# Optimization experiments

Measured on AMD Instinct MI355X. Metric: run time of the kernel, lower is better.

## Reference

```python
import jax, jax.numpy as jnp
import numpy as np

B, Q, K, H = 4, 128, 1024, 256
QS, KS, DV = 256, 256, 256


def setup_inputs() -> dict:
    key = jax.random.key(0)
    k1, k2, k3, k4, k5, k6, k7 = jax.random.split(key, 7)
    return {
        "queries": jax.random.normal(k1, (B, Q, QS), dtype=jnp.float32),
        "keys": jax.random.normal(k2, (B, K, KS), dtype=jnp.float32),
        "values": jax.random.normal(k3, (B, K, DV), dtype=jnp.float32),
        "valid_lens": jax.random.randint(k4, (B,), 1, K, dtype=jnp.int64),
        "Wq": jax.random.normal(k5, (QS, H), dtype=jnp.float32) / np.sqrt(QS),
        "Wk": jax.random.normal(k6, (KS, H), dtype=jnp.float32) / np.sqrt(KS),
        "Wv": jax.random.normal(k7, (H,), dtype=jnp.float32) / np.sqrt(H),
    }


def reference(queries, keys, values, valid_lens, Wq, Wk, Wv):
    # Projections: [B,Q,H] and [B,K,H]
    q = jnp.einsum("bqe,eh->bqh", queries, Wq)
    k = jnp.einsum("bke,eh->bkh", keys, Wk)
    # Broadcast add + tanh: [B,Q,K,H] intermediate (the kernel-headroom op)
    feats = jnp.tanh(q[:, :, None, :] + k[:, None, :, :])
    # hidden -> 1 reduction: scores [B,Q,K]
    scores = jnp.einsum("bqkh,h->bqk", feats, Wv)
    # masked softmax: positions >= valid_len set to -1e6 (as in sequence_mask)
    mask = jnp.arange(scores.shape[-1])[None, None, :] < valid_lens[:, None, None]
    scores = jnp.where(mask, scores, jnp.float32(-1e6))
    attn = jax.nn.softmax(scores, axis=-1)
    # dropout is identity in eval mode
    return jnp.einsum("bqk,bkv->bqv", attn, values)
```

## Files before the change

### kernel.cpp

```cpp
#include <hip/hip_runtime.h>

#define NB 4
#define NQ 128
#define NK 1024
#define NH 256
#define NE 256
#define NV 256

#define TSCALE     2.8853900817779268f
#define NEG2LOG2E -2.8853900817779268f

static __device__ __forceinline__ float fexp2(float x){ return __builtin_amdgcn_exp2f(x); }
static __device__ __forceinline__ float frcp (float x){ return __builtin_amdgcn_rcpf(x); }
static __device__ __forceinline__ float expT(float x){ return fexp2(x * TSCALE); }

__global__ __launch_bounds__(256) void proj_kernel(
    const float* __restrict__ qin, const float* __restrict__ kin,
    const float* __restrict__ Wq, const float* __restrict__ Wk,
    float4* __restrict__ qEa, float4* __restrict__ kEt) {
    const int tid = threadIdx.x;
    const int bi  = blockIdx.x;
    __shared__ float tr[NH][5];
    if (bi < NB * 32) {
        const int row0 = bi * 4;
        const float* r0 = qin + row0 * NE;
        float a0 = 0.f, a1 = 0.f, a2 = 0.f, a3 = 0.f;
#pragma unroll 2
        for (int e = 0; e < NE; e += 4) {
            float4 q0 = *(const float4*)(r0 + e);
            float4 q1 = *(const float4*)(r0 + NE + e);
            float4 q2 = *(const float4*)(r0 + 2 * NE + e);
            float4 q3 = *(const float4*)(r0 + 3 * NE + e);
#pragma unroll
            for (int j = 0; j < 4; ++j) {
                float w = Wq[(e + j) * NH + tid];
                a0 = fmaf(((const float*)&q0)[j], w, a0);
                a1 = fmaf(((const float*)&q1)[j], w, a1);
                a2 = fmaf(((const float*)&q2)[j], w, a2);
                a3 = fmaf(((const float*)&q3)[j], w, a3);
            }
        }
        qEa[bi * NH + tid] = make_float4(expT(a0), expT(a1),
                                         expT(a2), expT(a3));
    } else {
        const int kb = bi - NB * 32;
        const int b  = kb >> 8;
        const int k0 = (kb & 255) * 4;
        const int c   = k0 >> 6;
        const int kl0 = k0 & 63;
        const float* kr = kin + (b * NK + k0) * NE;
        float acc[4] = {0.f,0.f,0.f,0.f};
#pragma unroll 2
        for (int e = 0; e < NE; e += 4) {
            float4 kvv[4];
#pragma unroll
            for (int i = 0; i < 4; ++i) kvv[i] = *(const float4*)(kr + i * NE + e);
#pragma unroll
            for (int j = 0; j < 4; ++j) {
                float w = Wk[(e + j) * NH + tid];
#pragma unroll
                for (int i = 0; i < 4; ++i)
                    acc[i] = fmaf(((const float*)&kvv[i])[j], w, acc[i]);
            }
        }
#pragma unroll
        for (int i = 0; i < 4; ++i) tr[tid][i] = expT(acc[i]);
        __syncthreads();
        {
            const int hg = tid >> 2;
            const int kk = tid & 3;
            float4 v = make_float4(tr[hg*4+0][kk], tr[hg*4+1][kk],
                                   tr[hg*4+2][kk], tr[hg*4+3][kk]);
            kEt[((b * 16 + c) * 64 + hg) * 64 + kl0 + kk] = v;
        }
    }
}

__global__ __launch_bounds__(256) void attn_kernel(
    const float4* __restrict__ qEa,
    const float4* __restrict__ kEt, const float* __restrict__ V,
    const int* __restrict__ vlen, const float4* __restrict__ Wv4,
    float* __restrict__ part_s, float* __restrict__ part_pv) {
    const int tid = threadIdx.x, lane = tid & 63, wvid = tid >> 6;
    const int n0 = (vlen[0] + 63) >> 6, n1 = (vlen[1] + 63) >> 6;
    const int n2 = (vlen[2] + 63) >> 6, n3 = (vlen[3] + 63) >> 6;
    const int G  = n0 + n1 + n2 + n3;
    const int bi = blockIdx.x;
    const int xcd = bi & 7;
    const int jj  = bi >> 3;
    const int qq  = jj & 31;
    const int gs  = ((jj >> 5) << 3) + xcd;
    if (gs >= G) return;
    int b, chunk;
    if      (gs < n0)           { b = 0; chunk = gs; }
    else if (gs < n0 + n1)      { b = 1; chunk = gs - n0; }
    else if (gs < n0 + n1 + n2) { b = 2; chunk = gs - n0 - n1; }
    else                        { b = 3; chunk = gs - n0 - n1 - n2; }
    const int vl    = vlen[b];
    const int k0    = chunk * 64;
    const int k     = k0 + lane;
    const int pidx  = (b * 32 + qq) * 16 + chunk;
    float* ps  = part_s + pidx * 4;
    float* ppv = part_pv + pidx * (4 * NV);

    __shared__ float red17[4][64 * 17];
    __shared__ float pwT[64][4];

    const float4* kp = kEt + ((b * 16 + chunk) * 64 + wvid * 16) * 64 + lane;
    const float4* qp = qEa + (b * 32 + qq) * NH;
    float acc0 = 0.f, acc1 = 0.f, acc2 = 0.f, acc3 = 0.f;
#pragma unroll
    for (int i = 0; i < 16; ++i) {
        float4 kv4 = kp[i * 64];
        const int h4 = wvid * 16 + i;
        float4 wv4 = Wv4[h4];
#pragma unroll
        for (int j = 0; j < 4; ++j) {
            float kv  = (j==0)?kv4.x:(j==1)?kv4.y:(j==2)?kv4.z:kv4.w;
            float wvj = (j==0)?wv4.x:(j==1)?wv4.y:(j==2)?wv4.z:wv4.w;
            float4 qa = qp[h4 * 4 + j];
            float t0 = fmaf(qa.x, kv, 1.0f);
            float t1 = fmaf(qa.y, kv, 1.0f);
            float t2 = fmaf(qa.z, kv, 1.0f);
            float t3 = fmaf(qa.w, kv, 1.0f);
            float ab = t0 * t1, cd = t2 * t3;
            float rw = wvj * frcp(ab * cd);
            float rab = rw * cd, rcd = rw * ab;
            acc0 = fmaf(rab, t1, acc0);
            acc1 = fmaf(rab, t0, acc1);
            acc2 = fmaf(rcd, t3, acc2);
            acc3 = fmaf(rcd, t2, acc3);
        }
    }
    {
        float* hp = &red17[wvid][lane * 17];
        hp[0] = acc0; hp[1] = acc1; hp[2] = acc2; hp[3] = acc3;
    }
    __syncthreads();
    {
        const int row = wvid;
        float s = red17[0][lane * 17 + row] + red17[1][lane * 17 + row]
                + red17[2][lane * 17 + row] + red17[3][lane * 17 + row];
        float x = s * NEG2LOG2E;
        x = (k < vl) ? x : -1e38f;
        float p = fexp2(x);
        float u = p;
#pragma unroll
        for (int d = 32; d >= 1; d >>= 1) u += __shfl_xor(u, d, 64);
        if (lane == 0) ps[row] = u;
        pwT[lane][row] = p;
    }
    __syncthreads();
    {
        const float* Vb = V + (b * NK + k0) * NV;
        const int v4 = lane * 4;
        float4 o0 = {0,0,0,0}, o1 = {0,0,0,0}, o2 = {0,0,0,0}, o3 = {0,0,0,0};
#pragma unroll 4
        for (int kk = 0; kk < 16; ++kk) {
            const int kkk = wvid * 16 + kk;
            float4 pv = *(const float4*)&pwT[kkk][0];
            float4 vv = *(const float4*)&Vb[kkk * NV + v4];
            o0.x = fmaf(pv.x, vv.x, o0.x); o0.y = fmaf(pv.x, vv.y, o0.y);
            o0.z = fmaf(pv.x, vv.z, o0.z); o0.w = fmaf(pv.x, vv.w, o0.w);
            o1.x = fmaf(pv.y, vv.x, o1.x); o1.y = fmaf(pv.y, vv.y, o1.y);
            o1.z = fmaf(pv.y, vv.z, o1.z); o1.w = fmaf(pv.y, vv.w, o1.w);
            o2.x = fmaf(pv.z, vv.x, o2.x); o2.y = fmaf(pv.z, vv.y, o2.y);
            o2.z = fmaf(pv.z, vv.z, o2.z); o2.w = fmaf(pv.z, vv.w, o2.w);
            o3.x = fmaf(pv.w, vv.x, o3.x); o3.y = fmaf(pv.w, vv.y, o3.y);
            o3.z = fmaf(pv.w, vv.z, o3.z); o3.w = fmaf(pv.w, vv.w, o3.w);
        }
        float* pd = &red17[wvid][lane * 17];
        *(float4*)(pd + 0)  = o0;
        *(float4*)(pd + 4)  = o1;
        *(float4*)(pd + 8)  = o2;
        *(float4*)(pd + 12) = o3;
    }
    __syncthreads();
    {
        const int row = tid >> 6, vg = tid & 63;
        float4 r = {0,0,0,0};
#pragma unroll
        for (int ww = 0; ww < 4; ++ww) {
            float4 t = *(const float4*)&red17[ww][vg * 17 + row * 4];
            r.x += t.x; r.y += t.y; r.z += t.z; r.w += t.w;
        }
        *(float4*)&ppv[row * NV + vg * 4] = r;
    }
}

__global__ __launch_bounds__(256) void combine_kernel(
    const float* __restrict__ part_s, const float* __restrict__ part_pv,
    const int* __restrict__ vlen, float* __restrict__ out) {
    const int tid = threadIdx.x;
    const int idx = blockIdx.x;
    const int bi  = idx >> 2;
    const int i   = idx & 3;
    const int b   = bi >> 5;
    const int nb  = (vlen[b] + 63) >> 6;
    const int base = bi * 16;
    float S = 0.f, o = 0.f;
    for (int q = 0; q < nb; ++q) {
        S += part_s[(base + q) * 4 + i];
        o += part_pv[((base + q) * 4 + i) * NV + tid];
    }
    out[(bi * 4 + i) * NV + tid] = o * frcp(S);
}

extern "C" void kernel_launch(void* const* d_in, const int* in_sizes, int n_in,
                              void* d_out, int out_size, void* d_ws, size_t ws_size,
                              hipStream_t stream) {
    const float* queries = (const float*)d_in[0];
    const float* keys    = (const float*)d_in[1];
    const float* values  = (const float*)d_in[2];
    const int*   vlens   = (const int*)  d_in[3];
    const float* Wq      = (const float*)d_in[4];
    const float* Wk      = (const float*)d_in[5];
    const float* Wv      = (const float*)d_in[6];
    float* out = (float*)d_out;

    float4* qEa    = (float4*)d_ws;
    float4* kEt    = qEa + NB * 32 * NH;
    float*  part_s = (float*)(kEt + NB * 64 * NK);
    float*  part_pv = part_s + 8192;

    proj_kernel   <<<dim3(1152), dim3(256), 0, stream>>>(queries, keys, Wq, Wk,
                                                         qEa, kEt);
    attn_kernel   <<<dim3(2048), dim3(256), 0, stream>>>(qEa, kEt, values,
                                                         vlens, (const float4*)Wv,
                                                         part_s, part_pv);
    combine_kernel<<<dim3(512), dim3(256), 0, stream>>>(part_s, part_pv,
                                                        vlens, out);
}
```

Measured before the change: 112.5 us.

## Fuse combine into attention via last-block atomic counter; widen key projection tiles

Removes the separate combine kernel. The last attention block to finish for each (batch, query-group) now does the cross-chunk reduction itself, detected with an atomic counter that the projection kernel zeroes. The key projection also computes 8 keys per block instead of 4, so fewer blocks are launched and each Wk load is reused across more rows. This saves one kernel launch and its tail, at the cost of threadfences, atomics and a serialized reduction inside the tail blocks. The larger tile also raises register pressure.

```diff
diff --git a/kernel.cpp b/kernel.cpp
--- a/kernel.cpp
+++ b/kernel.cpp
@@ -17,10 +17,12 @@
 __global__ __launch_bounds__(256) void proj_kernel(
     const float* __restrict__ qin, const float* __restrict__ kin,
     const float* __restrict__ Wq, const float* __restrict__ Wk,
-    float4* __restrict__ qEa, float4* __restrict__ kEt) {
+    float4* __restrict__ qEa, float4* __restrict__ kEt,
+    int* __restrict__ cnt) {
     const int tid = threadIdx.x;
     const int bi  = blockIdx.x;
-    __shared__ float tr[NH][5];
+    __shared__ float tr[NH][9];
+    if (bi == 0 && tid < NB * 32) cnt[tid] = 0;
     if (bi < NB * 32) {
         const int row0 = bi * 4;
         const float* r0 = qin + row0 * NE;
@@ -44,31 +46,33 @@
                                          expT(a2), expT(a3));
     } else {
         const int kb = bi - NB * 32;
-        const int b  = kb >> 8;
-        const int k0 = (kb & 255) * 4;
+        const int b  = kb >> 7;
+        const int k0 = (kb & 127) * 8;
         const int c   = k0 >> 6;
         const int kl0 = k0 & 63;
         const float* kr = kin + (b * NK + k0) * NE;
-        float acc[4] = {0.f,0.f,0.f,0.f};
+        float acc[8] = {0.f,0.f,0.f,0.f,0.f,0.f,0.f,0.f};
 #pragma unroll 2
         for (int e = 0; e < NE; e += 4) {
-            float4 kvv[4];
-#pragma unroll
-            for (int i = 0; i < 4; ++i) kvv[i] = *(const float4*)(kr + i * NE + e);
+            float4 kvv[8];
+#pragma unroll
+            for (int i = 0; i < 8; ++i) kvv[i] = *(const float4*)(kr + i * NE + e);
 #pragma unroll
             for (int j = 0; j < 4; ++j) {
                 float w = Wk[(e + j) * NH + tid];
 #pragma unroll
-                for (int i = 0; i < 4; ++i)
+                for (int i = 0; i < 8; ++i)
                     acc[i] = fmaf(((const float*)&kvv[i])[j], w, acc[i]);
             }
         }
 #pragma unroll
-        for (int i = 0; i < 4; ++i) tr[tid][i] = expT(acc[i]);
+        for (int i = 0; i < 8; ++i) tr[tid][i] = expT(acc[i]);
         __syncthreads();
-        {
-            const int hg = tid >> 2;
-            const int kk = tid & 3;
+#pragma unroll
+        for (int p = 0; p < 2; ++p) {
+            int idx2 = p * 256 + tid;
+            int hg = idx2 >> 3;
+            int kk = idx2 & 7;
             float4 v = make_float4(tr[hg*4+0][kk], tr[hg*4+1][kk],
                                    tr[hg*4+2][kk], tr[hg*4+3][kk]);
             kEt[((b * 16 + c) * 64 + hg) * 64 + kl0 + kk] = v;
@@ -80,7 +84,8 @@
     const float4* __restrict__ qEa,
     const float4* __restrict__ kEt, const float* __restrict__ V,
     const int* __restrict__ vlen, const float4* __restrict__ Wv4,
-    float* __restrict__ part_s, float* __restrict__ part_pv) {
+    float* __restrict__ part_s, float* __restrict__ part_pv,
+    int* __restrict__ cnt, float* __restrict__ out) {
     const int tid = threadIdx.x, lane = tid & 63, wvid = tid >> 6;
     const int n0 = (vlen[0] + 63) >> 6, n1 = (vlen[1] + 63) >> 6;
     const int n2 = (vlen[2] + 63) >> 6, n3 = (vlen[3] + 63) >> 6;
@@ -97,17 +102,20 @@
     else if (gs < n0 + n1 + n2) { b = 2; chunk = gs - n0 - n1; }
     else                        { b = 3; chunk = gs - n0 - n1 - n2; }
     const int vl    = vlen[b];
+    const int nb    = (vl + 63) >> 6;
     const int k0    = chunk * 64;
     const int k     = k0 + lane;
-    const int pidx  = (b * 32 + qq) * 16 + chunk;
+    const int bq    = b * 32 + qq;
+    const int pidx  = bq * 16 + chunk;
     float* ps  = part_s + pidx * 4;
     float* ppv = part_pv + pidx * (4 * NV);
 
     __shared__ float red17[4][64 * 17];
     __shared__ float pwT[64][4];
+    __shared__ int lastFlag;
 
     const float4* kp = kEt + ((b * 16 + chunk) * 64 + wvid * 16) * 64 + lane;
-    const float4* qp = qEa + (b * 32 + qq) * NH;
+    const float4* qp = qEa + bq * NH;
     float acc0 = 0.f, acc1 = 0.f, acc2 = 0.f, acc3 = 0.f;
 #pragma unroll
     for (int i = 0; i < 16; ++i) {
@@ -186,24 +194,27 @@
         }
         *(float4*)&ppv[row * NV + vg * 4] = r;
     }
-}
-
-__global__ __launch_bounds__(256) void combine_kernel(
-    const float* __restrict__ part_s, const float* __restrict__ part_pv,
-    const int* __restrict__ vlen, float* __restrict__ out) {
-    const int tid = threadIdx.x;
-    const int idx = blockIdx.x;
-    const int bi  = idx >> 2;
-    const int i   = idx & 3;
-    const int b   = bi >> 5;
-    const int nb  = (vlen[b] + 63) >> 6;
-    const int base = bi * 16;
-    float S = 0.f, o = 0.f;
-    for (int q = 0; q < nb; ++q) {
-        S += part_s[(base + q) * 4 + i];
-        o += part_pv[((base + q) * 4 + i) * NV + tid];
-    }
-    out[(bi * 4 + i) * NV + tid] = o * frcp(S);
+    __syncthreads();
+    __threadfence();
+    if (tid == 0) {
+        int old = atomicAdd(&cnt[bq], 1);
+        lastFlag = (old == nb - 1);
+    }
+    __syncthreads();
+    if (!lastFlag) return;
+    __threadfence();
+    {
+        const int base = bq * 16;
+#pragma unroll
+        for (int i = 0; i < 4; ++i) {
+            float S = 0.f, o = 0.f;
+            for (int q = 0; q < nb; ++q) {
+                S += part_s[(base + q) * 4 + i];
+                o += part_pv[((base + q) * 4 + i) * NV + tid];
+            }
+            out[(bq * 4 + i) * NV + tid] = o * frcp(S);
+        }
+    }
 }
 
 extern "C" void kernel_launch(void* const* d_in, const int* in_sizes, int n_in,
@@ -222,12 +233,11 @@
     float4* kEt    = qEa + NB * 32 * NH;
     float*  part_s = (float*)(kEt + NB * 64 * NK);
     float*  part_pv = part_s + 8192;
-
-    proj_kernel   <<<dim3(1152), dim3(256), 0, stream>>>(queries, keys, Wq, Wk,
-                                                         qEa, kEt);
-    attn_kernel   <<<dim3(2048), dim3(256), 0, stream>>>(qEa, kEt, values,
-                                                         vlens, (const float4*)Wv,
-                                                         part_s, part_pv);
-    combine_kernel<<<dim3(512), dim3(256), 0, stream>>>(part_s, part_pv,
-                                                        vlens, out);
+    int*    cnt    = (int*)(part_pv + 2 * 1024 * 1024);
+
+    proj_kernel<<<dim3(640), dim3(256), 0, stream>>>(queries, keys, Wq, Wk,
+                                                     qEa, kEt, cnt);
+    attn_kernel<<<dim3(2048), dim3(256), 0, stream>>>(qEa, kEt, values,
+                                                      vlens, (const float4*)Wv,
+                                                      part_s, part_pv, cnt, out);
 }
```

After: 245.3 us. 118% more time.
